# Optimization experiments

Measured on AMD Instinct MI355X. Metric: run time of the kernel, lower is better.

The kernel has to match this reference:

```python
import jax, jax.numpy as jnp
import numpy as np

HIDDEN = 1024
HEADS = 16
HEAD_DIM = HIDDEN // HEADS


def setup_inputs() -> dict:
    key = jax.random.key(0)
    ks = jax.random.split(key, 11)
    B, T, S, D = 4, 2048, 2048, HIDDEN
    sc = 1.0 / np.sqrt(D)
    return {
        "query": jax.random.normal(ks[0], (B, T, D), jnp.float32),
        "key": jax.random.normal(ks[1], (B, S, D), jnp.float32),
        "value": jax.random.normal(ks[2], (B, S, D), jnp.float32),
        "Wq": jax.random.normal(ks[3], (D, D), jnp.float32) * sc,
        "bq": jnp.zeros((D,), jnp.float32),
        "Wk": jax.random.normal(ks[4], (D, D), jnp.float32) * sc,
        "bk": jnp.zeros((D,), jnp.float32),
        "Wv": jax.random.normal(ks[5], (D, D), jnp.float32) * sc,
        "bv": jnp.zeros((D,), jnp.float32),
        "Wo": jax.random.normal(ks[6], (D, D), jnp.float32) * sc,
        "bo": jnp.zeros((D,), jnp.float32),
    }


def reference(query, key, value, Wq, bq, Wk, bk, Wv, bv, Wo, bo):
    B, T, D = query.shape
    S = key.shape[1]
    H, hd = HEADS, HEAD_DIM
    q = (query @ Wq + bq).reshape(B, T, H, hd)
    k = (key @ Wk + bk).reshape(B, S, H, hd)
    v = (value @ Wv + bv).reshape(B, S, H, hd)
    # scores: [B, H, T, S]
    scores = jnp.einsum("bthd,bshd->bhts", q, k) / np.sqrt(hd).astype(q.dtype)
    attn = jax.nn.softmax(scores, axis=-1)
    out = jnp.einsum("bhts,bshd->bthd", attn, v).reshape(B, T, D)
    return out @ Wo + bo
```

## Files before the change

### kernel.cpp

```cpp
#include <hip/hip_runtime.h>
#include <cstdint>
#include <cstddef>


typedef __bf16 bf16x8 __attribute__((ext_vector_type(8)));
typedef float  f32x4  __attribute__((ext_vector_type(4)));
typedef unsigned short ushort_t;

#define DEV __device__ __forceinline__

DEV ushort_t f2bf(float f) {
  unsigned int u = __builtin_bit_cast(unsigned int, f);
  u = u + 0x7fffu + ((u >> 16) & 1u);
  return (ushort_t)(u >> 16);
}
DEV float bf2f(ushort_t b) {
  unsigned int u = ((unsigned int)b) << 16;
  return __builtin_bit_cast(float, u);
}
DEV bf16x8 ld16(const ushort_t* p) { return *(const bf16x8*)p; }

DEV void gload_lds16(const void* g, void* l) {
  __builtin_amdgcn_global_load_lds(
      (__attribute__((address_space(1))) void*)(void*)g,
      (__attribute__((address_space(3))) void*)l, 16, 0, 0);
}

__global__ void cvt_kernel(const float* __restrict__ in, ushort_t* __restrict__ out, int n4) {
  int i = blockIdx.x * blockDim.x + threadIdx.x;
  const int stride = gridDim.x * blockDim.x;
  for (; i < n4; i += stride) {
    const float4 v = ((const float4*)in)[i];
    ushort4 o;
    o.x = f2bf(v.x); o.y = f2bf(v.y); o.z = f2bf(v.z); o.w = f2bf(v.w);
    ((ushort4*)out)[i] = o;
  }
}

__global__ void transpose_cvt_kernel(const float* __restrict__ W, ushort_t* __restrict__ Wt) {
  __shared__ float tile[32][33];
  const int c0 = blockIdx.x * 32, r0 = blockIdx.y * 32;
  const int x = threadIdx.x, y0 = threadIdx.y;
#pragma unroll
  for (int yy = 0; yy < 32; yy += 8)
    tile[y0 + yy][x] = W[(size_t)(r0 + y0 + yy) * 1024 + c0 + x];
  __syncthreads();
#pragma unroll
  for (int yy = 0; yy < 32; yy += 8)
    Wt[(size_t)(c0 + y0 + yy) * 1024 + r0 + x] = f2bf(tile[x][y0 + yy]);
}

template <int OUTMODE>
__global__ __launch_bounds__(256)
void gemm_kernel(const ushort_t* __restrict__ A, const ushort_t* __restrict__ Bt,
                 const float* __restrict__ bias, void* __restrict__ Cout) {
  constexpr int K = 1024, N = 1024;
  __shared__ __attribute__((aligned(16))) ushort_t As[128 * 32];
  __shared__ __attribute__((aligned(16))) ushort_t Bs[128 * 32];
  const int tid = threadIdx.x;
  const int l = tid & 63, w = tid >> 6;
  const int l15 = l & 15, lg = l >> 4;
  const int bm = blockIdx.x >> 3, bn = blockIdx.x & 7;
  const int m0 = bm << 7, n0 = bn << 7;
  const int wm = (w >> 1) << 6, wn = (w & 1) << 6;

  f32x4 acc[4][4];
#pragma unroll
  for (int i = 0; i < 4; ++i)
#pragma unroll
    for (int j = 0; j < 4; ++j) acc[i][j] = f32x4{0.f, 0.f, 0.f, 0.f};

  const int srow = tid >> 2, slot = tid & 3;
  const ushort_t* aS0 = A + (size_t)(m0 + srow) * K + slot * 8;
  const ushort_t* aS1 = aS0 + (size_t)64 * K;
  const ushort_t* bS0 = Bt + (size_t)(n0 + srow) * K + slot * 8;
  const ushort_t* bS1 = bS0 + (size_t)64 * K;
  ushort_t* aD0 = As + tid * 8;  ushort_t* aD1 = aD0 + 2048;
  ushort_t* bD0 = Bs + tid * 8;  ushort_t* bD1 = bD0 + 2048;

  const int aoff = (wm + l15) * 32 + lg * 8;
  const int boff = (wn + l15) * 32 + lg * 8;

  for (int k0 = 0; k0 < K; k0 += 32) {
    gload_lds16(aS0 + k0, aD0);
    gload_lds16(aS1 + k0, aD1);
    gload_lds16(bS0 + k0, bD0);
    gload_lds16(bS1 + k0, bD1);
    __syncthreads();
    bf16x8 af[4], bfr[4];
#pragma unroll
    for (int i = 0; i < 4; ++i) af[i] = *(const bf16x8*)(As + aoff + i * 512);
#pragma unroll
    for (int j = 0; j < 4; ++j) bfr[j] = *(const bf16x8*)(Bs + boff + j * 512);
#pragma unroll
    for (int i = 0; i < 4; ++i)
#pragma unroll
      for (int j = 0; j < 4; ++j)
        acc[i][j] = __builtin_amdgcn_mfma_f32_16x16x32_bf16(af[i], bfr[j], acc[i][j], 0, 0, 0);
    __syncthreads();
  }

#pragma unroll
  for (int i = 0; i < 4; ++i) {
    const int grow0 = m0 + wm + i * 16 + lg * 4;
#pragma unroll
    for (int j = 0; j < 4; ++j) {
      const int gcol = n0 + wn + j * 16 + l15;
      const float bj = bias[gcol];
#pragma unroll
      for (int r = 0; r < 4; ++r) {
        const float v = acc[i][j][r] + bj;
        const int grow = grow0 + r;
        if constexpr (OUTMODE == 0) {
          ((ushort_t*)Cout)[(size_t)grow * N + gcol] = f2bf(v);
        } else if constexpr (OUTMODE == 1) {
          const int bb = grow >> 11, t = grow & 2047;
          const int h = gcol >> 6, d = gcol & 63;
          ((ushort_t*)Cout)[((size_t)((bb * 16 + h) * 64 + d) << 11) + t] = f2bf(v);
        } else {
          ((float*)Cout)[(size_t)grow * N + gcol] = v;
        }
      }
    }
  }
}

__global__ __launch_bounds__(256)
void attn_kernel(const ushort_t* __restrict__ Qp, const ushort_t* __restrict__ Kp,
                 const ushort_t* __restrict__ Vt, ushort_t* __restrict__ AO) {
  __shared__ __attribute__((aligned(16))) ushort_t Ks[2][4096];
  __shared__ __attribute__((aligned(16))) ushort_t Vs[2][4096];
  __shared__ __attribute__((aligned(16))) ushort_t Pl[4][2048];

  const int tid = threadIdx.x;
  const int l = tid & 63, wid = tid >> 6;
  const int l15 = l & 15, lg = l >> 4;
  const int bh = blockIdx.x >> 4, qt = blockIdx.x & 15;
  const int b = bh >> 4, h = bh & 15;
  const int q0 = qt * 128 + wid * 32;

  const int srow = tid >> 3;
  const int slot = tid & 7;
  const int sslot = slot ^ (srow & 7);
  const ushort_t* kS = Kp + (size_t)(b * 2048 + srow) * 1024 + h * 64 + sslot * 8;
  const ushort_t* vS = Vt + ((size_t)((b * 16 + h) * 64 + srow)) * 2048 + sslot * 8;
  ushort_t* kD = &Ks[0][0] + tid * 8;
  ushort_t* vD = &Vs[0][0] + tid * 8;

#define STAGE(buf, s0)                                                        \
  do {                                                                        \
    gload_lds16(kS + (size_t)(s0) * 1024, kD + (buf) * 4096);                 \
    gload_lds16(kS + (size_t)((s0) + 32) * 1024, kD + (buf) * 4096 + 2048);   \
    gload_lds16(vS + (s0), vD + (buf) * 4096);                                \
    gload_lds16(vS + (size_t)32 * 2048 + (s0), vD + (buf) * 4096 + 2048);     \
  } while (0)

  const ushort_t* qptr = Qp + (size_t)(b * 2048 + q0 + l15) * 1024 + h * 64 + lg * 8;
  bf16x8 qf[2][2];
  qf[0][0] = ld16(qptr);              qf[0][1] = ld16(qptr + 32);
  qf[1][0] = ld16(qptr + 16 * 1024);  qf[1][1] = ld16(qptr + 16 * 1024 + 32);

  ushort_t* myP = &Pl[wid][0];

  f32x4 o[2][4];
  float mrow[2][4], lrow[2][4];
#pragma unroll
  for (int mf = 0; mf < 2; ++mf) {
#pragma unroll
    for (int hf = 0; hf < 4; ++hf) o[mf][hf] = f32x4{0.f, 0.f, 0.f, 0.f};
#pragma unroll
    for (int r = 0; r < 4; ++r) { mrow[mf][r] = -1e30f; lrow[mf][r] = 0.f; }
  }

  STAGE(0, 0);

  for (int sb = 0; sb < 32; ++sb) {
    const int cur = sb & 1;
    if (sb < 31) {
      STAGE(cur ^ 1, (sb + 1) * 64);
      asm volatile("s_waitcnt vmcnt(4)" ::: "memory");
    } else {
      asm volatile("s_waitcnt vmcnt(0)" ::: "memory");
    }
    __builtin_amdgcn_s_barrier();

    const ushort_t* kb = &Ks[cur][0];
    const ushort_t* vb = &Vs[cur][0];

    bf16x8 kf[4][2];
#pragma unroll
    for (int cf = 0; cf < 4; ++cf)
#pragma unroll
      for (int kk = 0; kk < 2; ++kk) {
        const int row = cf * 16 + l15;
        kf[cf][kk] = ld16(kb + row * 64 + ((kk * 4 + lg) ^ (row & 7)) * 8);
      }
    f32x4 sf[2][4];
#pragma unroll
    for (int mf = 0; mf < 2; ++mf)
#pragma unroll
      for (int cf = 0; cf < 4; ++cf) {
        f32x4 a = f32x4{0.f, 0.f, 0.f, 0.f};
        a = __builtin_amdgcn_mfma_f32_16x16x32_bf16(qf[mf][0], kf[cf][0], a, 0, 0, 0);
        a = __builtin_amdgcn_mfma_f32_16x16x32_bf16(qf[mf][1], kf[cf][1], a, 0, 0, 0);
        sf[mf][cf] = a * 0.125f;
      }

#pragma unroll
    for (int mf = 0; mf < 2; ++mf) {
      float bmax[4];
#pragma unroll
      for (int r = 0; r < 4; ++r)
        bmax[r] = fmaxf(fmaxf(sf[mf][0][r], sf[mf][1][r]),
                        fmaxf(sf[mf][2][r], sf[mf][3][r]));
#pragma unroll
      for (int m = 1; m < 16; m <<= 1)
#pragma unroll
        for (int r = 0; r < 4; ++r) bmax[r] = fmaxf(bmax[r], __shfl_xor(bmax[r], m));
      float sc[4];
#pragma unroll
      for (int r = 0; r < 4; ++r) {
        const float mn = fmaxf(mrow[mf][r], bmax[r]);
        sc[r] = __expf(mrow[mf][r] - mn);
        mrow[mf][r] = mn;
        lrow[mf][r] *= sc[r];
      }
#pragma unroll
      for (int hf = 0; hf < 4; ++hf)
#pragma unroll
        for (int r = 0; r < 4; ++r) o[mf][hf][r] *= sc[r];
#pragma unroll
      for (int cf = 0; cf < 4; ++cf)
#pragma unroll
        for (int r = 0; r < 4; ++r) {
          const float p = __expf(sf[mf][cf][r] - mrow[mf][r]);
          const ushort_t pb = f2bf(p);
          lrow[mf][r] += bf2f(pb);
          const int row = mf * 16 + lg * 4 + r;
          myP[row * 64 + ((cf * 16 + l15) ^ ((row & 7) << 3))] = pb;
        }
    }
    asm volatile("s_waitcnt lgkmcnt(0)" ::: "memory");
    __builtin_amdgcn_sched_barrier(0);

    bf16x8 pf[2][2], vf[4][2];
#pragma unroll
    for (int mf = 0; mf < 2; ++mf)
#pragma unroll
      for (int ks = 0; ks < 2; ++ks) {
        const int row = mf * 16 + l15;
        pf[mf][ks] = ld16(myP + row * 64 + ((ks * 4 + lg) ^ (row & 7)) * 8);
      }
#pragma unroll
    for (int hf = 0; hf < 4; ++hf)
#pragma unroll
      for (int ks = 0; ks < 2; ++ks) {
        const int row = hf * 16 + l15;
        vf[hf][ks] = ld16(vb + row * 64 + ((ks * 4 + lg) ^ (row & 7)) * 8);
      }
#pragma unroll
    for (int mf = 0; mf < 2; ++mf)
#pragma unroll
      for (int hf = 0; hf < 4; ++hf) {
        o[mf][hf] = __builtin_amdgcn_mfma_f32_16x16x32_bf16(pf[mf][0], vf[hf][0], o[mf][hf], 0, 0, 0);
        o[mf][hf] = __builtin_amdgcn_mfma_f32_16x16x32_bf16(pf[mf][1], vf[hf][1], o[mf][hf], 0, 0, 0);
      }

    asm volatile("s_waitcnt lgkmcnt(0)" ::: "memory");
    __builtin_amdgcn_s_barrier();
  }
#undef STAGE

#pragma unroll
  for (int mf = 0; mf < 2; ++mf) {
#pragma unroll
    for (int m = 1; m < 16; m <<= 1)
#pragma unroll
      for (int r = 0; r < 4; ++r) lrow[mf][r] += __shfl_xor(lrow[mf][r], m);
    float linv[4];
#pragma unroll
    for (int r = 0; r < 4; ++r) linv[r] = 1.f / lrow[mf][r];
#pragma unroll
    for (int hf = 0; hf < 4; ++hf)
#pragma unroll
      for (int r = 0; r < 4; ++r)
        AO[(size_t)(b * 2048 + q0 + mf * 16 + lg * 4 + r) * 1024 + h * 64 + hf * 16 + l15] =
            f2bf(o[mf][hf][r] * linv[r]);
  }
}

extern "C" void kernel_launch(void* const* d_in, const int* in_sizes, int n_in,
                              void* d_out, int out_size, void* d_ws, size_t ws_size,
                              hipStream_t stream) {
  (void)in_sizes; (void)n_in; (void)out_size;
  const float* query = (const float*)d_in[0];
  const float* key   = (const float*)d_in[1];
  const float* value = (const float*)d_in[2];
  const float* Wq = (const float*)d_in[3]; const float* bq = (const float*)d_in[4];
  const float* Wk = (const float*)d_in[5]; const float* bk = (const float*)d_in[6];
  const float* Wv = (const float*)d_in[7]; const float* bv = (const float*)d_in[8];
  const float* Wo = (const float*)d_in[9]; const float* bo = (const float*)d_in[10];
  float* out = (float*)d_out;

  constexpr size_t SZX = (size_t)8192 * 1024;
  constexpr size_t SZW = (size_t)1024 * 1024;
  constexpr size_t NEEDED = (7 * SZX + 4 * SZW) * sizeof(ushort_t);
  if (ws_size < NEEDED) return;

  ushort_t* p = (ushort_t*)d_ws;
  ushort_t* Xq = p;  p += SZX;
  ushort_t* Xk = p;  p += SZX;
  ushort_t* Xv = p;  p += SZX;
  ushort_t* Qp = p;  p += SZX;
  ushort_t* Kp = p;  p += SZX;
  ushort_t* Vt = p;  p += SZX;
  ushort_t* AO = p;  p += SZX;
  ushort_t* Wqt = p; p += SZW;
  ushort_t* Wkt = p; p += SZW;
  ushort_t* Wvt = p; p += SZW;
  ushort_t* Wot = p; p += SZW;

  const int n4 = (int)(SZX / 4);
  cvt_kernel<<<dim3(2048), dim3(256), 0, stream>>>(query, Xq, n4);
  cvt_kernel<<<dim3(2048), dim3(256), 0, stream>>>(key,   Xk, n4);
  cvt_kernel<<<dim3(2048), dim3(256), 0, stream>>>(value, Xv, n4);

  dim3 tg(32, 32), tb(32, 8);
  transpose_cvt_kernel<<<tg, tb, 0, stream>>>(Wq, Wqt);
  transpose_cvt_kernel<<<tg, tb, 0, stream>>>(Wk, Wkt);
  transpose_cvt_kernel<<<tg, tb, 0, stream>>>(Wv, Wvt);
  transpose_cvt_kernel<<<tg, tb, 0, stream>>>(Wo, Wot);

  gemm_kernel<0><<<dim3(512), dim3(256), 0, stream>>>(Xq, Wqt, bq, (void*)Qp);
  gemm_kernel<0><<<dim3(512), dim3(256), 0, stream>>>(Xk, Wkt, bk, (void*)Kp);
  gemm_kernel<1><<<dim3(512), dim3(256), 0, stream>>>(Xv, Wvt, bv, (void*)Vt);

  attn_kernel<<<dim3(1024), dim3(256), 0, stream>>>(Qp, Kp, Vt, AO);

  gemm_kernel<2><<<dim3(512), dim3(256), 0, stream>>>(AO, Wot, bo, (void*)out);
}
```

Measured before the change: 484.2 us.

## Keep softmax probabilities in registers via transposed MFMA and lane shuffles

The attention kernel now computes S^T (K as the A operand) so that each lane holds a full query column. The row max and row sum then need only two cross-lane shuffles, and P is packed to bf16 with v_cvt_pk_bf16 and rearranged into PV MFMA operands through xor-shuffles, which removes the LDS round trip and its waitcnt. The 1/sqrt(d) scale is folded into the Q projection GEMM epilogue, s_setprio brackets are added around the MFMA blocks, and the output store is vectorised to ushort4. The added risk is correctness of the shuffle permutation and a slight precision change from the running sum now using unrounded fp32 p.

Result: faster. 422.5 us (-12.7%).

```diff
diff --git a/kernel.cpp b/kernel.cpp
--- a/kernel.cpp
+++ b/kernel.cpp
@@ -5,6 +5,7 @@
 
 typedef __bf16 bf16x8 __attribute__((ext_vector_type(8)));
 typedef float  f32x4  __attribute__((ext_vector_type(4)));
+typedef uint32_t u32x4 __attribute__((ext_vector_type(4)));
 typedef unsigned short ushort_t;
 
 #define DEV __device__ __forceinline__
@@ -14,9 +15,10 @@
   u = u + 0x7fffu + ((u >> 16) & 1u);
   return (ushort_t)(u >> 16);
 }
-DEV float bf2f(ushort_t b) {
-  unsigned int u = ((unsigned int)b) << 16;
-  return __builtin_bit_cast(float, u);
+DEV uint32_t cvt_pk_bf16(float lo, float hi) {
+  uint32_t r;
+  asm("v_cvt_pk_bf16_f32 %0, %1, %2" : "=v"(r) : "v"(lo), "v"(hi));
+  return r;
 }
 DEV bf16x8 ld16(const ushort_t* p) { return *(const bf16x8*)p; }
 
@@ -53,7 +55,7 @@
 template <int OUTMODE>
 __global__ __launch_bounds__(256)
 void gemm_kernel(const ushort_t* __restrict__ A, const ushort_t* __restrict__ Bt,
-                 const float* __restrict__ bias, void* __restrict__ Cout) {
+                 const float* __restrict__ bias, float scale, void* __restrict__ Cout) {
   constexpr int K = 1024, N = 1024;
   __shared__ __attribute__((aligned(16))) ushort_t As[128 * 32];
   __shared__ __attribute__((aligned(16))) ushort_t Bs[128 * 32];
@@ -109,7 +111,7 @@
       const float bj = bias[gcol];
 #pragma unroll
       for (int r = 0; r < 4; ++r) {
-        const float v = acc[i][j][r] + bj;
+        const float v = (acc[i][j][r] + bj) * scale;
         const int grow = grow0 + r;
         if constexpr (OUTMODE == 0) {
           ((ushort_t*)Cout)[(size_t)grow * N + gcol] = f2bf(v);
@@ -130,11 +132,12 @@
                  const ushort_t* __restrict__ Vt, ushort_t* __restrict__ AO) {
   __shared__ __attribute__((aligned(16))) ushort_t Ks[2][4096];
   __shared__ __attribute__((aligned(16))) ushort_t Vs[2][4096];
-  __shared__ __attribute__((aligned(16))) ushort_t Pl[4][2048];
 
   const int tid = threadIdx.x;
   const int l = tid & 63, wid = tid >> 6;
   const int l15 = l & 15, lg = l >> 4;
+  const int b1 = (lg >> 1) & 1, b0 = lg & 1;
+  const bool diag = (b0 == b1);
   const int bh = blockIdx.x >> 4, qt = blockIdx.x & 15;
   const int b = bh >> 4, h = bh & 15;
   const int q0 = qt * 128 + wid * 32;
@@ -160,17 +163,13 @@
   qf[0][0] = ld16(qptr);              qf[0][1] = ld16(qptr + 32);
   qf[1][0] = ld16(qptr + 16 * 1024);  qf[1][1] = ld16(qptr + 16 * 1024 + 32);
 
-  ushort_t* myP = &Pl[wid][0];
-
   f32x4 o[2][4];
-  float mrow[2][4], lrow[2][4];
-#pragma unroll
-  for (int mf = 0; mf < 2; ++mf) {
-#pragma unroll
-    for (int hf = 0; hf < 4; ++hf) o[mf][hf] = f32x4{0.f, 0.f, 0.f, 0.f};
-#pragma unroll
-    for (int r = 0; r < 4; ++r) { mrow[mf][r] = -1e30f; lrow[mf][r] = 0.f; }
-  }
+  float mrun[2] = {-1e30f, -1e30f};
+  float lrun[2] = {0.f, 0.f};
+#pragma unroll
+  for (int qh = 0; qh < 2; ++qh)
+#pragma unroll
+    for (int hf = 0; hf < 4; ++hf) o[qh][hf] = f32x4{0.f, 0.f, 0.f, 0.f};
 
   STAGE(0, 0);
 
@@ -195,62 +194,80 @@
         const int row = cf * 16 + l15;
         kf[cf][kk] = ld16(kb + row * 64 + ((kk * 4 + lg) ^ (row & 7)) * 8);
       }
-    f32x4 sf[2][4];
-#pragma unroll
-    for (int mf = 0; mf < 2; ++mf)
+    f32x4 st[2][4];
+    __builtin_amdgcn_s_setprio(1);
+#pragma unroll
+    for (int qh = 0; qh < 2; ++qh)
 #pragma unroll
       for (int cf = 0; cf < 4; ++cf) {
         f32x4 a = f32x4{0.f, 0.f, 0.f, 0.f};
-        a = __builtin_amdgcn_mfma_f32_16x16x32_bf16(qf[mf][0], kf[cf][0], a, 0, 0, 0);
-        a = __builtin_amdgcn_mfma_f32_16x16x32_bf16(qf[mf][1], kf[cf][1], a, 0, 0, 0);
-        sf[mf][cf] = a * 0.125f;
-      }
-
-#pragma unroll
-    for (int mf = 0; mf < 2; ++mf) {
-      float bmax[4];
-#pragma unroll
-      for (int r = 0; r < 4; ++r)
-        bmax[r] = fmaxf(fmaxf(sf[mf][0][r], sf[mf][1][r]),
-                        fmaxf(sf[mf][2][r], sf[mf][3][r]));
-#pragma unroll
-      for (int m = 1; m < 16; m <<= 1)
-#pragma unroll
-        for (int r = 0; r < 4; ++r) bmax[r] = fmaxf(bmax[r], __shfl_xor(bmax[r], m));
-      float sc[4];
-#pragma unroll
-      for (int r = 0; r < 4; ++r) {
-        const float mn = fmaxf(mrow[mf][r], bmax[r]);
-        sc[r] = __expf(mrow[mf][r] - mn);
-        mrow[mf][r] = mn;
-        lrow[mf][r] *= sc[r];
-      }
-#pragma unroll
-      for (int hf = 0; hf < 4; ++hf)
-#pragma unroll
-        for (int r = 0; r < 4; ++r) o[mf][hf][r] *= sc[r];
+        a = __builtin_amdgcn_mfma_f32_16x16x32_bf16(kf[cf][0], qf[qh][0], a, 0, 0, 0);
+        a = __builtin_amdgcn_mfma_f32_16x16x32_bf16(kf[cf][1], qf[qh][1], a, 0, 0, 0);
+        st[qh][cf] = a;
+      }
+    __builtin_amdgcn_s_setprio(0);
+
+    bf16x8 pfrag[2][2];
+#pragma unroll
+    for (int qh = 0; qh < 2; ++qh) {
+      float bm = st[qh][0][0];
 #pragma unroll
       for (int cf = 0; cf < 4; ++cf)
 #pragma unroll
+        for (int r = 0; r < 4; ++r) bm = fmaxf(bm, st[qh][cf][r]);
+      bm = fmaxf(bm, __shfl_xor(bm, 16));
+      bm = fmaxf(bm, __shfl_xor(bm, 32));
+      const float mn = fmaxf(mrun[qh], bm);
+      const float sc = __expf(mrun[qh] - mn);
+      mrun[qh] = mn;
+      float ls = 0.f;
+#pragma unroll
+      for (int cf = 0; cf < 4; ++cf)
+#pragma unroll
         for (int r = 0; r < 4; ++r) {
-          const float p = __expf(sf[mf][cf][r] - mrow[mf][r]);
-          const ushort_t pb = f2bf(p);
-          lrow[mf][r] += bf2f(pb);
-          const int row = mf * 16 + lg * 4 + r;
-          myP[row * 64 + ((cf * 16 + l15) ^ ((row & 7) << 3))] = pb;
+          const float p = __expf(st[qh][cf][r] - mn);
+          st[qh][cf][r] = p;
+          ls += p;
         }
+      lrun[qh] = lrun[qh] * sc + ls;
+#pragma unroll
+      for (int hf = 0; hf < 4; ++hf) o[qh][hf] *= sc;
+
+      uint32_t u[4][2];
+#pragma unroll
+      for (int cf = 0; cf < 4; ++cf)
+#pragma unroll
+        for (int tp = 0; tp < 2; ++tp)
+          u[cf][tp] = cvt_pk_bf16(st[qh][cf][2 * tp], st[qh][cf][2 * tp + 1]);
+
+      uint32_t r1[4], keep[4];
+#pragma unroll
+      for (int cfh = 0; cfh < 2; ++cfh)
+#pragma unroll
+        for (int tp = 0; tp < 2; ++tp) {
+          const uint32_t snd = b1 ? u[2 * cfh][tp] : u[2 * cfh + 1][tp];
+          r1[cfh * 2 + tp] = (uint32_t)__shfl_xor((int)snd, 32);
+          keep[cfh * 2 + tp] = b1 ? u[2 * cfh + 1][tp] : u[2 * cfh][tp];
+        }
+      uint32_t w[4], stay[4];
+#pragma unroll
+      for (int i = 0; i < 4; ++i) {
+        const uint32_t z = diag ? r1[i] : keep[i];
+        w[i] = (uint32_t)__shfl_xor((int)z, 16);
+        stay[i] = diag ? keep[i] : r1[i];
+      }
+#pragma unroll
+      for (int ks = 0; ks < 2; ++ks) {
+        u32x4 bb;
+        bb.x = b0 ? w[2 * ks]     : stay[2 * ks];
+        bb.y = b0 ? w[2 * ks + 1] : stay[2 * ks + 1];
+        bb.z = b0 ? stay[2 * ks]     : w[2 * ks];
+        bb.w = b0 ? stay[2 * ks + 1] : w[2 * ks + 1];
+        pfrag[qh][ks] = __builtin_bit_cast(bf16x8, bb);
+      }
     }
-    asm volatile("s_waitcnt lgkmcnt(0)" ::: "memory");
-    __builtin_amdgcn_sched_barrier(0);
-
-    bf16x8 pf[2][2], vf[4][2];
-#pragma unroll
-    for (int mf = 0; mf < 2; ++mf)
-#pragma unroll
-      for (int ks = 0; ks < 2; ++ks) {
-        const int row = mf * 16 + l15;
-        pf[mf][ks] = ld16(myP + row * 64 + ((ks * 4 + lg) ^ (row & 7)) * 8);
-      }
+
+    bf16x8 vf[4][2];
 #pragma unroll
     for (int hf = 0; hf < 4; ++hf)
 #pragma unroll
@@ -258,13 +275,15 @@
         const int row = hf * 16 + l15;
         vf[hf][ks] = ld16(vb + row * 64 + ((ks * 4 + lg) ^ (row & 7)) * 8);
       }
-#pragma unroll
-    for (int mf = 0; mf < 2; ++mf)
+    __builtin_amdgcn_s_setprio(1);
+#pragma unroll
+    for (int qh = 0; qh < 2; ++qh)
 #pragma unroll
       for (int hf = 0; hf < 4; ++hf) {
-        o[mf][hf] = __builtin_amdgcn_mfma_f32_16x16x32_bf16(pf[mf][0], vf[hf][0], o[mf][hf], 0, 0, 0);
-        o[mf][hf] = __builtin_amdgcn_mfma_f32_16x16x32_bf16(pf[mf][1], vf[hf][1], o[mf][hf], 0, 0, 0);
-      }
+        o[qh][hf] = __builtin_amdgcn_mfma_f32_16x16x32_bf16(vf[hf][0], pfrag[qh][0], o[qh][hf], 0, 0, 0);
+        o[qh][hf] = __builtin_amdgcn_mfma_f32_16x16x32_bf16(vf[hf][1], pfrag[qh][1], o[qh][hf], 0, 0, 0);
+      }
+    __builtin_amdgcn_s_setprio(0);
 
     asm volatile("s_waitcnt lgkmcnt(0)" ::: "memory");
     __builtin_amdgcn_s_barrier();
@@ -272,20 +291,21 @@
 #undef STAGE
 
 #pragma unroll
-  for (int mf = 0; mf < 2; ++mf) {
-#pragma unroll
-    for (int m = 1; m < 16; m <<= 1)
-#pragma unroll
-      for (int r = 0; r < 4; ++r) lrow[mf][r] += __shfl_xor(lrow[mf][r], m);
-    float linv[4];
-#pragma unroll
-    for (int r = 0; r < 4; ++r) linv[r] = 1.f / lrow[mf][r];
-#pragma unroll
-    for (int hf = 0; hf < 4; ++hf)
-#pragma unroll
-      for (int r = 0; r < 4; ++r)
-        AO[(size_t)(b * 2048 + q0 + mf * 16 + lg * 4 + r) * 1024 + h * 64 + hf * 16 + l15] =
-            f2bf(o[mf][hf][r] * linv[r]);
+  for (int qh = 0; qh < 2; ++qh) {
+    float lr = lrun[qh];
+    lr += __shfl_xor(lr, 16);
+    lr += __shfl_xor(lr, 32);
+    const float linv = 1.f / lr;
+    const size_t rbase = (size_t)(b * 2048 + q0 + qh * 16 + l15) * 1024 + h * 64 + lg * 4;
+#pragma unroll
+    for (int hf = 0; hf < 4; ++hf) {
+      ushort4 pk;
+      pk.x = f2bf(o[qh][hf][0] * linv);
+      pk.y = f2bf(o[qh][hf][1] * linv);
+      pk.z = f2bf(o[qh][hf][2] * linv);
+      pk.w = f2bf(o[qh][hf][3] * linv);
+      *(ushort4*)(AO + rbase + hf * 16) = pk;
+    }
   }
 }
 
@@ -331,11 +351,11 @@
   transpose_cvt_kernel<<<tg, tb, 0, stream>>>(Wv, Wvt);
   transpose_cvt_kernel<<<tg, tb, 0, stream>>>(Wo, Wot);
 
-  gemm_kernel<0><<<dim3(512), dim3(256), 0, stream>>>(Xq, Wqt, bq, (void*)Qp);
-  gemm_kernel<0><<<dim3(512), dim3(256), 0, stream>>>(Xk, Wkt, bk, (void*)Kp);
-  gemm_kernel<1><<<dim3(512), dim3(256), 0, stream>>>(Xv, Wvt, bv, (void*)Vt);
+  gemm_kernel<0><<<dim3(512), dim3(256), 0, stream>>>(Xq, Wqt, bq, 0.125f, (void*)Qp);
+  gemm_kernel<0><<<dim3(512), dim3(256), 0, stream>>>(Xk, Wkt, bk, 1.0f,   (void*)Kp);
+  gemm_kernel<1><<<dim3(512), dim3(256), 0, stream>>>(Xv, Wvt, bv, 1.0f,   (void*)Vt);
 
   attn_kernel<<<dim3(1024), dim3(256), 0, stream>>>(Qp, Kp, Vt, AO);
 
-  gemm_kernel<2><<<dim3(512), dim3(256), 0, stream>>>(AO, Wot, bo, (void*)out);
-}
+  gemm_kernel<2><<<dim3(512), dim3(256), 0, stream>>>(AO, Wot, bo, 1.0f, (void*)out);
+}
```
